# Performance work log

Hardware: AMD Instinct MI355X
Metric: run time of the kernel (lower is better)

The kernel has to match this reference:

```python
import jax, jax.numpy as jnp
import numpy as np

N_NODES = 100000
N_EDGES = 640000
HIDDEN = 128


def setup_inputs() -> dict:
    key = jax.random.key(0)
    k1, k2, k3, k4 = jax.random.split(key, 4)
    node_emb = jax.random.normal(k1, (N_NODES, HIDDEN), dtype=jnp.float32)
    edge_index = jax.random.randint(k2, (2, N_EDGES), 0, N_NODES, dtype=jnp.int64)
    # edge head params: Linear(2H -> H), Linear(H -> 2)
    s1 = 1.0 / np.sqrt(2 * HIDDEN)
    s2 = 1.0 / np.sqrt(HIDDEN)
    W1 = jax.random.uniform(k3, (2 * HIDDEN, HIDDEN), jnp.float32, -s1, s1)
    b1 = jnp.zeros((HIDDEN,), jnp.float32)
    W2 = jax.random.uniform(k4, (HIDDEN, 2), jnp.float32, -s2, s2)
    b2 = jnp.zeros((2,), jnp.float32)
    return {"node_emb": node_emb, "edge_index": edge_index,
            "W1": W1, "b1": b1, "W2": W2, "b2": b2}


def reference(node_emb, edge_index, W1, b1, W2, b2):
    # gather src/dst node embeddings by edge_index (irregular gather)
    src, dst = edge_index[0], edge_index[1]
    edge_emb = jnp.concatenate([node_emb[src], node_emb[dst]], axis=-1)  # [E, 2H]
    # edge head: Linear -> ReLU -> (Dropout = identity in eval) -> Linear
    h = jax.nn.relu(edge_emb @ W1 + b1)  # [E, H]
    flow_pred = h @ W2 + b2              # [E, 2]
    return flow_pred
```

## Files before the change

### kernel.cpp

```cpp
#include <hip/hip_runtime.h>

typedef __attribute__((ext_vector_type(8))) short short8;
typedef __attribute__((ext_vector_type(4))) short short4v;
typedef __attribute__((ext_vector_type(4))) float floatx4;
typedef __attribute__((ext_vector_type(2))) float floatx2;

static __device__ __forceinline__ unsigned short f2bf(float f) {
    union { float f; unsigned int u; } v; v.f = f;
    unsigned int u = v.u;
    return (unsigned short)((u + 0x7FFFu + ((u >> 16) & 1u)) >> 16);
}
static __device__ __forceinline__ float bf2f(short x) {
    return __uint_as_float(((unsigned int)(unsigned short)x) << 16);
}

__global__ void cvt_wt_kernel(const float* __restrict__ w1,
                              unsigned short* __restrict__ wt) {
    __shared__ unsigned short sT[32 * 130];
    const int b = blockIdx.x;
    const int kg0 = b * 32;
    const int h = (kg0 >= 128) ? 1 : 0;
    const int kk0 = kg0 & 127;
    const int tid = threadIdx.x;
#pragma unroll
    for (int i = 0; i < 16; i++) {
        int idx = tid + i * 256;
        int k = idx >> 7, n = idx & 127;
        sT[k * 130 + n] = f2bf(w1[(kg0 + k) * 128 + n]);
    }
    __syncthreads();
#pragma unroll
    for (int i = 0; i < 16; i++) {
        int idx = tid + i * 256;
        int n = idx >> 5, k = idx & 31;
        wt[(h * 128 + n) * 128 + kk0 + k] = sT[k * 130 + n];
    }
}

__global__ __launch_bounds__(512, 4) void node_gemm_kernel(
    float* xy,
    const unsigned short* __restrict__ wt,
    const float* __restrict__ b1, int N)
{
    __shared__ unsigned short sW[256 * 128];

    const int tid = threadIdx.x;
    const int lane = tid & 63, wave = tid >> 6;
    const int l15 = lane & 15, lq = lane >> 4;

#pragma unroll
    for (int i = 0; i < 8; i++) {
        int u = tid + i * 512;
        int r = u >> 4, s = u & 15;
        *(short8*)&sW[r * 128 + ((s ^ r) & 15) * 8] =
            *(const short8*)&wt[r * 128 + s * 8];
    }
    __syncthreads();

    const int nr = blockIdx.x * 128 + wave * 16 + l15;
    const int nc = (nr < N) ? nr : (N - 1);
    const float* xrow = xy + (size_t)nc * 128;

    floatx4 acc[16];
#pragma unroll
    for (int mt = 0; mt < 16; mt++) acc[mt] = (floatx4){0.f, 0.f, 0.f, 0.f};

#pragma unroll
    for (int kh = 0; kh < 2; kh++) {
        float4 xf[4];
#pragma unroll
        for (int q = 0; q < 4; q++)
            xf[q] = *(const float4*)(xrow + kh * 64 + (q >> 1) * 32 + lq * 8
                                     + (q & 1) * 4);
        short8 bf[2];
#pragma unroll
        for (int t = 0; t < 2; t++) {
            bf[t][0] = (short)f2bf(xf[2 * t].x);
            bf[t][1] = (short)f2bf(xf[2 * t].y);
            bf[t][2] = (short)f2bf(xf[2 * t].z);
            bf[t][3] = (short)f2bf(xf[2 * t].w);
            bf[t][4] = (short)f2bf(xf[2 * t + 1].x);
            bf[t][5] = (short)f2bf(xf[2 * t + 1].y);
            bf[t][6] = (short)f2bf(xf[2 * t + 1].z);
            bf[t][7] = (short)f2bf(xf[2 * t + 1].w);
        }
#pragma unroll
        for (int t = 0; t < 2; t++) {
            const int ks = kh * 2 + t;
#pragma unroll
            for (int mt = 0; mt < 16; mt++) {
                const short8 af = *(const short8*)
                    &sW[(mt * 16 + l15) * 128 + (((ks * 4 + lq) ^ l15) & 15) * 8];
                acc[mt] = __builtin_amdgcn_mfma_f32_16x16x32_bf16(af, bf[t],
                                                                  acc[mt], 0, 0, 0);
            }
        }
    }

    if (nr < N) {
        unsigned short* yrow = (unsigned short*)xy + (size_t)nr * 256;
#pragma unroll
        for (int mt = 0; mt < 16; mt++) {
            const int oc = mt * 16 + lq * 4;
            float4 bb = (mt < 8) ? *(const float4*)&b1[oc]
                                 : (float4){0.f, 0.f, 0.f, 0.f};
            short4v pk;
            pk[0] = (short)f2bf(acc[mt][0] + bb.x);
            pk[1] = (short)f2bf(acc[mt][1] + bb.y);
            pk[2] = (short)f2bf(acc[mt][2] + bb.z);
            pk[3] = (short)f2bf(acc[mt][3] + bb.w);
            *(short4v*)(yrow + oc) = pk;
        }
    }
}

__global__ __launch_bounds__(256) void edge_kernel(
    const unsigned short* __restrict__ Y,
    const int* __restrict__ eidx,
    const float* __restrict__ w2,
    const float* __restrict__ b2,
    float* __restrict__ out,
    int E, int n_nodes)
{
    const int tid = threadIdx.x;
    const int lane = tid & 63, wave = tid >> 6;
    const int r = lane >> 4, cl = lane & 15;

    float w20[8], w21[8];
#pragma unroll
    for (int q = 0; q < 4; q++) {
        const float4 f = *(const float4*)&w2[cl * 16 + q * 4];
        w20[q * 2]     = f.x; w21[q * 2]     = f.y;
        w20[q * 2 + 1] = f.z; w21[q * 2 + 1] = f.w;
    }
    const float bb0 = b2[0], bb1 = b2[1];

    const long eb = (long)blockIdx.x * 256 + wave * 64;
    const char* Yb = (const char*)Y;

    int sg[4], dg[4];
    short8 buf[2][2][4];

#define LOAD_IDX(CH)                                                        \
    _Pragma("unroll")                                                       \
    for (int g = 0; g < 4; g++) {                                           \
        long e = eb + (CH) * 16 + g * 4 + r; if (e >= E) e = E - 1;         \
        int s = __builtin_nontemporal_load(&eidx[e]);                       \
        int d = __builtin_nontemporal_load(&eidx[(long)E + e]);             \
        sg[g] = (s < 0) ? 0 : (s >= n_nodes ? n_nodes - 1 : s);             \
        dg[g] = (d < 0) ? 0 : (d >= n_nodes ? n_nodes - 1 : d);             \
    }
#define LOAD_Y(P)                                                           \
    _Pragma("unroll")                                                       \
    for (int g = 0; g < 4; g++) {                                           \
        buf[P][0][g] = *(const short8*)(Yb + (size_t)sg[g] * 512 + cl * 16);\
        buf[P][1][g] = *(const short8*)(Yb + (size_t)dg[g] * 512 + 256      \
                                        + cl * 16);                         \
    }

    LOAD_IDX(0); LOAD_Y(0);
    LOAD_IDX(1); LOAD_Y(1);

    for (int ch = 0; ch < 4; ch++) {
        const int p = ch & 1;
        if (ch < 2) { LOAD_IDX(ch + 2); }
#pragma unroll
        for (int g = 0; g < 4; g++) {
            float p0 = 0.f, p1 = 0.f;
#pragma unroll
            for (int j = 0; j < 8; j++) {
                float f = bf2f(buf[p][0][g][j]) + bf2f(buf[p][1][g][j]);
                f = fmaxf(f, 0.f);
                p0 = fmaf(f, w20[j], p0);
                p1 = fmaf(f, w21[j], p1);
            }
#pragma unroll
            for (int m = 1; m < 16; m <<= 1) {
                p0 += __shfl_xor(p0, m, 64);
                p1 += __shfl_xor(p1, m, 64);
            }
            if (cl == 0) {
                const long e = eb + ch * 16 + g * 4 + r;
                if (e < E) {
                    floatx2 o;
                    o.x = p0 + bb0; o.y = p1 + bb1;
                    __builtin_nontemporal_store(o, (floatx2*)&out[e * 2]);
                }
            }
        }
        if (ch < 2) { LOAD_Y(p); }
    }
#undef LOAD_IDX
#undef LOAD_Y
}

extern "C" void kernel_launch(void* const* d_in, const int* in_sizes, int n_in,
                              void* d_out, int out_size, void* d_ws, size_t ws_size,
                              hipStream_t stream) {
    float*       xy   = (float*)d_in[0];
    const int*   eidx = (const int*)d_in[1];
    const float* W1   = (const float*)d_in[2];
    const float* b1   = (const float*)d_in[3];
    const float* W2   = (const float*)d_in[4];
    const float* b2   = (const float*)d_in[5];
    float* out = (float*)d_out;

    const int n_node_elems = in_sizes[0];
    const int N = n_node_elems / 128;
    const int E = in_sizes[1] / 2;

    unsigned short* wt = (unsigned short*)d_ws;

    cvt_wt_kernel<<<8, 256, 0, stream>>>(W1, wt);

    const int nblk1 = (N + 127) / 128;
    node_gemm_kernel<<<nblk1, 512, 0, stream>>>(xy, wt, b1, N);

    const int nblk2 = (E + 255) / 256;
    edge_kernel<<<nblk2, 256, 0, stream>>>((const unsigned short*)xy, eidx,
                                           W2, b2, out, E, N);
}
```

Measured before the change: 163.5 us.

## Keep W1 slices in registers and stage node tile in LDS

The node GEMM is restructured so each wave holds a 64-column slice of the transposed bf16 weights in registers, loaded straight from global memory. The block's 128-row node tile is converted to bf16 and staged in swizzled LDS. This drops the 64KB per-block weight copy into LDS, halving shared memory to 32KB and raising possible occupancy. The cost is more register pressure and repeated weight loads from L2 by every wave. The in-place overwrite of the node rows stays safe because of the barrier after staging.

```diff
diff --git a/kernel.cpp b/kernel.cpp
--- a/kernel.cpp
+++ b/kernel.cpp
@@ -42,74 +42,68 @@
     const unsigned short* __restrict__ wt,
     const float* __restrict__ b1, int N)
 {
-    __shared__ unsigned short sW[256 * 128];
+    __shared__ unsigned short sX[128 * 128];
 
     const int tid = threadIdx.x;
     const int lane = tid & 63, wave = tid >> 6;
     const int l15 = lane & 15, lq = lane >> 4;
+    const int row0 = blockIdx.x * 128;
+
+    const int cs = wave & 3;
+    short8 af[4][4];
+#pragma unroll
+    for (int mt = 0; mt < 4; mt++)
+#pragma unroll
+        for (int ks = 0; ks < 4; ks++)
+            af[mt][ks] = *(const short8*)
+                &wt[(cs * 64 + mt * 16 + l15) * 128 + ks * 32 + lq * 8];
 
 #pragma unroll
     for (int i = 0; i < 8; i++) {
         int u = tid + i * 512;
-        int r = u >> 4, s = u & 15;
-        *(short8*)&sW[r * 128 + ((s ^ r) & 15) * 8] =
-            *(const short8*)&wt[r * 128 + s * 8];
+        int n = u >> 5, f4 = u & 31;
+        int rr = row0 + n; if (rr >= N) rr = N - 1;
+        const float4 xv = *(const float4*)(xy + (size_t)rr * 128 + f4 * 4);
+        short4v pk;
+        pk[0] = (short)f2bf(xv.x); pk[1] = (short)f2bf(xv.y);
+        pk[2] = (short)f2bf(xv.z); pk[3] = (short)f2bf(xv.w);
+        int s = f4 >> 1, hh = f4 & 1;
+        *(short4v*)&sX[n * 128 + ((s ^ (n & 15)) * 16 + hh * 8) / 2] = pk;
     }
     __syncthreads();
 
-    const int nr = blockIdx.x * 128 + wave * 16 + l15;
-    const int nc = (nr < N) ? nr : (N - 1);
-    const float* xrow = xy + (size_t)nc * 128;
-
-    floatx4 acc[16];
-#pragma unroll
-    for (int mt = 0; mt < 16; mt++) acc[mt] = (floatx4){0.f, 0.f, 0.f, 0.f};
-
-#pragma unroll
-    for (int kh = 0; kh < 2; kh++) {
-        float4 xf[4];
-#pragma unroll
-        for (int q = 0; q < 4; q++)
-            xf[q] = *(const float4*)(xrow + kh * 64 + (q >> 1) * 32 + lq * 8
-                                     + (q & 1) * 4);
-        short8 bf[2];
-#pragma unroll
-        for (int t = 0; t < 2; t++) {
-            bf[t][0] = (short)f2bf(xf[2 * t].x);
-            bf[t][1] = (short)f2bf(xf[2 * t].y);
-            bf[t][2] = (short)f2bf(xf[2 * t].z);
-            bf[t][3] = (short)f2bf(xf[2 * t].w);
-            bf[t][4] = (short)f2bf(xf[2 * t + 1].x);
-            bf[t][5] = (short)f2bf(xf[2 * t + 1].y);
-            bf[t][6] = (short)f2bf(xf[2 * t + 1].z);
-            bf[t][7] = (short)f2bf(xf[2 * t + 1].w);
+    const int rt0 = wave >> 2;
+#pragma unroll
+    for (int j = 0; j < 4; j++) {
+        const int rt = rt0 + j * 2;
+        floatx4 acc[4];
+#pragma unroll
+        for (int mt = 0; mt < 4; mt++) acc[mt] = (floatx4){0.f, 0.f, 0.f, 0.f};
+#pragma unroll
+        for (int ks = 0; ks < 4; ks++) {
+            const int n = rt * 16 + l15;
+            const short8 bf = *(const short8*)
+                &sX[n * 128 + (((ks * 4 + lq) ^ l15) & 15) * 8];
+#pragma unroll
+            for (int mt = 0; mt < 4; mt++)
+                acc[mt] = __builtin_amdgcn_mfma_f32_16x16x32_bf16(
+                    af[mt][ks], bf, acc[mt], 0, 0, 0);
         }
-#pragma unroll
-        for (int t = 0; t < 2; t++) {
-            const int ks = kh * 2 + t;
-#pragma unroll
-            for (int mt = 0; mt < 16; mt++) {
-                const short8 af = *(const short8*)
-                    &sW[(mt * 16 + l15) * 128 + (((ks * 4 + lq) ^ l15) & 15) * 8];
-                acc[mt] = __builtin_amdgcn_mfma_f32_16x16x32_bf16(af, bf[t],
-                                                                  acc[mt], 0, 0, 0);
-            }
-        }
-    }
-
-    if (nr < N) {
-        unsigned short* yrow = (unsigned short*)xy + (size_t)nr * 256;
-#pragma unroll
-        for (int mt = 0; mt < 16; mt++) {
-            const int oc = mt * 16 + lq * 4;
-            float4 bb = (mt < 8) ? *(const float4*)&b1[oc]
-                                 : (float4){0.f, 0.f, 0.f, 0.f};
-            short4v pk;
-            pk[0] = (short)f2bf(acc[mt][0] + bb.x);
-            pk[1] = (short)f2bf(acc[mt][1] + bb.y);
-            pk[2] = (short)f2bf(acc[mt][2] + bb.z);
-            pk[3] = (short)f2bf(acc[mt][3] + bb.w);
-            *(short4v*)(yrow + oc) = pk;
+        const int nr = row0 + rt * 16 + l15;
+        if (nr < N) {
+            unsigned short* yrow = (unsigned short*)xy + (size_t)nr * 256;
+#pragma unroll
+            for (int mt = 0; mt < 4; mt++) {
+                const int oc = cs * 64 + mt * 16 + lq * 4;
+                float4 bb = (oc < 128) ? *(const float4*)&b1[oc]
+                                       : (float4){0.f, 0.f, 0.f, 0.f};
+                short4v pk;
+                pk[0] = (short)f2bf(acc[mt][0] + bb.x);
+                pk[1] = (short)f2bf(acc[mt][1] + bb.y);
+                pk[2] = (short)f2bf(acc[mt][2] + bb.z);
+                pk[3] = (short)f2bf(acc[mt][3] + bb.w);
+                *(short4v*)(yrow + oc) = pk;
+            }
         }
     }
 }
```

Measured after the change: 170.6 us. 1.04x slower.
